# Kernel tuning notes

Measured on AMD Instinct MI355X. Metric: run time of the kernel, lower is better.

## Reference

```python
import jax, jax.numpy as jnp
import numpy as np

D_MODEL = 512
D_STATE = 128
D_CONV = 4
EXPAND = 2
HEADDIM = 64
NLAYERS = 2
D_INNER = EXPAND * D_MODEL          # 1024
NHEADS = D_INNER // HEADDIM         # 16
CONV_DIM = D_INNER + 2 * D_STATE    # 1280 (x, B, C share the depthwise conv)
D_IN_PROJ = 2 * D_INNER + 2 * D_STATE + NHEADS  # 2320 (z, xBC, dt)
VOCAB = 40
SEQ = 64
BATCH = 512
NUM_CLASSES = 2
FC_HID = 128
EPS = 1e-5


def setup_inputs() -> dict:
    key = jax.random.key(0)
    ks = jax.random.split(key, 12)
    x = jax.random.randint(ks[0], (BATCH, SEQ), 0, VOCAB)
    emb = jax.random.uniform(ks[1], (VOCAB, D_MODEL), minval=-0.1, maxval=0.1)
    emb = emb.at[0].set(0.0)  # padding_idx=0
    pos = jax.random.normal(ks[2], (1, SEQ, D_MODEL)) * 0.02
    in_proj_w = jax.random.normal(ks[3], (NLAYERS, D_IN_PROJ, D_MODEL)) * 0.02
    conv_w = jax.random.normal(ks[4], (NLAYERS, CONV_DIM, D_CONV)) * 0.1
    conv_b = jnp.zeros((NLAYERS, CONV_DIM))
    dt0 = jax.random.uniform(ks[5], (NLAYERS, NHEADS), minval=1e-3, maxval=0.1)
    dt_bias = dt0 + jnp.log(-jnp.expm1(-dt0))  # inverse softplus of dt0
    A_log = jnp.log(jax.random.uniform(ks[6], (NLAYERS, NHEADS), minval=1.0, maxval=16.0))
    D_skip = jnp.ones((NLAYERS, NHEADS))
    norm_w = jnp.ones((NLAYERS, D_INNER))
    out_proj_w = jax.random.normal(ks[7], (NLAYERS, D_MODEL, D_INNER)) * 0.02
    ln_g = jnp.ones((NLAYERS, D_MODEL))
    ln_b = jnp.zeros((NLAYERS, D_MODEL))
    fc1_w = jax.random.uniform(ks[8], (FC_HID, D_MODEL), minval=-0.1, maxval=0.1)
    fc1_b = jnp.zeros((FC_HID,))
    fc2_w = jax.random.uniform(ks[9], (NUM_CLASSES, FC_HID), minval=-0.1, maxval=0.1)
    fc2_b = jnp.zeros((NUM_CLASSES,))
    return dict(x=x, emb=emb, pos=pos, in_proj_w=in_proj_w, conv_w=conv_w,
                conv_b=conv_b, dt_bias=dt_bias, A_log=A_log, D_skip=D_skip,
                norm_w=norm_w, out_proj_w=out_proj_w, ln_g=ln_g, ln_b=ln_b,
                fc1_w=fc1_w, fc1_b=fc1_b, fc2_w=fc2_w, fc2_b=fc2_b)


def _layernorm(h, g, b):
    mu = jnp.mean(h, axis=-1, keepdims=True)
    var = jnp.mean(jnp.square(h - mu), axis=-1, keepdims=True)
    return (h - mu) * jax.lax.rsqrt(var + EPS) * g + b


def _mamba2_block(h, in_proj_w, conv_w, conv_b, dt_bias, A_log, D_skip, norm_w, out_proj_w):
    b, s, _ = h.shape
    zxbcdt = jnp.einsum('bsd,ed->bse', h, in_proj_w)  # [b,s,D_IN_PROJ]
    z = zxbcdt[..., :D_INNER]
    xBC = zxbcdt[..., D_INNER:D_INNER + CONV_DIM]
    dt_raw = zxbcdt[..., D_INNER + CONV_DIM:]          # [b,s,NHEADS]
    # causal depthwise 1D conv + silu
    xBC_t = jnp.pad(jnp.swapaxes(xBC, 1, 2), ((0, 0), (0, 0), (D_CONV - 1, 0)))
    conv = jax.lax.conv_general_dilated(xBC_t, conv_w[:, None, :], (1,), 'VALID',
                                        feature_group_count=CONV_DIM)
    xBC = jax.nn.silu(jnp.swapaxes(conv + conv_b[None, :, None], 1, 2))
    xs = xBC[..., :D_INNER].reshape(b, s, NHEADS, HEADDIM)
    Bm = xBC[..., D_INNER:D_INNER + D_STATE]           # [b,s,n] (ngroups=1)
    Cm = xBC[..., D_INNER + D_STATE:]                  # [b,s,n]
    dt = jax.nn.softplus(dt_raw + dt_bias)             # [b,s,h]
    A = -jnp.exp(A_log)                                # [h], negative
    # exact quadratic (1-semiseparable) SSD form, equal to the selective scan
    cum = jnp.cumsum(dt * A, axis=1)                   # [b,s,h]
    diff = cum[:, :, None, :] - cum[:, None, :, :]     # [b,i,j,h] <= 0 for i>=j
    causal = jnp.tril(jnp.ones((s, s), dtype=bool))
    L = jnp.exp(jnp.where(causal[None, :, :, None], diff, -jnp.inf))  # decay mask
    scores = jnp.einsum('bin,bjn->bij', Cm, Bm)
    M = scores[..., None] * L                          # [b,i,j,h]
    y = jnp.einsum('bijh,bjh,bjhp->bihp', M, dt, xs)
    y = y + D_skip[None, None, :, None] * xs
    y = y.reshape(b, s, D_INNER)
    # gated RMSNorm
    y = y * jax.nn.silu(z)
    y = y * jax.lax.rsqrt(jnp.mean(jnp.square(y), axis=-1, keepdims=True) + EPS) * norm_w
    return jnp.einsum('bsi,di->bsd', y, out_proj_w)


def reference(x, emb, pos, in_proj_w, conv_w, conv_b, dt_bias, A_log, D_skip,
              norm_w, out_proj_w, ln_g, ln_b, fc1_w, fc1_b, fc2_w, fc2_b):
    h = emb[x] + pos[:, :x.shape[1], :]  # dropout is identity in eval
    for l in range(NLAYERS):
        y = _mamba2_block(h, in_proj_w[l], conv_w[l], conv_b[l], dt_bias[l],
                          A_log[l], D_skip[l], norm_w[l], out_proj_w[l])
        h = h + _layernorm(y, ln_g[l], ln_b[l])
    pm = (jnp.sum(h, axis=-1) != 0).astype(h.dtype)[..., None]  # [b,s,1]
    pooled = jnp.sum(h * pm, axis=1) / jnp.clip(jnp.sum(pm, axis=1), 1.0, None)
    hid = jax.nn.relu(pooled @ fc1_w.T + fc1_b)
    return hid @ fc2_w.T + fc2_b
```

## Files before the change

### kernel.cpp

```cpp
#include <hip/hip_runtime.h>
#include <hip/hip_bf16.h>

#define D_MODEL   512
#define D_STATE   128
#define D_CONV    4
#define HEADDIM   64
#define NLAYERS   2
#define D_INNER   1024
#define NHEADS    16
#define CONV_DIM  1280
#define D_IN_PROJ 2320
#define NPAD      2560
#define SEQ       64
#define BATCH     512
#define NTOK      (BATCH*SEQ)
#define FC_HID    128
#define EPS       1e-5f

using bf16 = __hip_bfloat16;
typedef __bf16 bf16x8 __attribute__((ext_vector_type(8)));
typedef float  f32x4  __attribute__((ext_vector_type(4)));

__device__ __forceinline__ float b2f(bf16 v)  { return __bfloat162float(v); }
__device__ __forceinline__ bf16  f2b(float v) { return __float2bfloat16(v); }
__device__ __forceinline__ float bflo(unsigned u){ return __builtin_bit_cast(float, u << 16); }
__device__ __forceinline__ float bfhi(unsigned u){ return __builtin_bit_cast(float, u & 0xffff0000u); }

__device__ __forceinline__ void gl_lds16(const void* g, void* l) {
    __builtin_amdgcn_global_load_lds((const __attribute__((address_space(1))) void*)g,
                                     (__attribute__((address_space(3))) void*)l, 16, 0, 0);
}

__global__ __launch_bounds__(256) void k_embed(const int* __restrict__ x,
        const float* __restrict__ emb, const float* __restrict__ pos,
        float* __restrict__ h, bf16* __restrict__ hb) {
    int idx = blockIdx.x*256 + threadIdx.x;
    int d   = (idx & 127) * 4;
    int tok = idx >> 7;
    int s   = tok & (SEQ-1);
    int v   = x[tok];
    float4 e4 = *(const float4*)(emb + (size_t)v*D_MODEL + d);
    float4 p4 = *(const float4*)(pos + (size_t)s*D_MODEL + d);
    float4 r; r.x=e4.x+p4.x; r.y=e4.y+p4.y; r.z=e4.z+p4.z; r.w=e4.w+p4.w;
    *(float4*)(h + (size_t)tok*D_MODEL + d) = r;
    bf16 o[4] = { f2b(r.x), f2b(r.y), f2b(r.z), f2b(r.w) };
    *(uint2*)(hb + (size_t)tok*D_MODEL + d) = *(uint2*)&o[0];
}

__global__ __launch_bounds__(256) void k_cvtw(const float* __restrict__ src,
        bf16* __restrict__ dst, int R, int Kc, int total8) {
    int idx = blockIdx.x*256 + threadIdx.x;
    if (idx >= total8) return;
    int e0 = idx*8;
    int r = e0 / Kc, c = e0 % Kc;
    bf16 tb[8];
    if (r < R) {
        float4 f0 = *(const float4*)(src + (size_t)r*Kc + c);
        float4 f1 = *(const float4*)(src + (size_t)r*Kc + c + 4);
        tb[0]=f2b(f0.x); tb[1]=f2b(f0.y); tb[2]=f2b(f0.z); tb[3]=f2b(f0.w);
        tb[4]=f2b(f1.x); tb[5]=f2b(f1.y); tb[6]=f2b(f1.z); tb[7]=f2b(f1.w);
    } else {
        #pragma unroll
        for (int e=0;e<8;e++) tb[e] = f2b(0.f);
    }
    *(uint4*)(dst + (size_t)r*Kc + c) = *(uint4*)&tb[0];
}

__global__ __launch_bounds__(512, 1) void k_gemm256(const bf16* __restrict__ A,
        const bf16* __restrict__ B, bf16* __restrict__ zbuf,
        bf16* __restrict__ xbcc, float* __restrict__ dt, float* __restrict__ cum,
        const float* __restrict__ cw, const float* __restrict__ cb,
        const float* __restrict__ dt_bias, const float* __restrict__ A_log,
        int ctok)
{
    constexpr int KDIM = 512, NT = KDIM/64, NBX = NPAD/256;
    extern __shared__ __align__(16) char lds[];
    bf16* Cs = (bf16*)lds;

    const int nwg = gridDim.x;
    const int q = nwg >> 3, r = nwg & 7;
    const int xcd = blockIdx.x & 7, loc = blockIdx.x >> 3;
    const int wg = ((xcd < r) ? xcd*(q+1) : r*(q+1) + (xcd-r)*q) + loc;
    const int m0 = (wg / NBX) * 256;
    const int n0 = (wg % NBX) * 256;

    const int t = threadIdx.x;
    const int wid = t >> 6, lane = t & 63;
    const int lr = lane & 15, lg = lane >> 4;
    const int wm = (wid >> 2)*128, wn = (wid & 3)*64;
    const int srow = wid*32;
    const int sr   = lane >> 3;
    const int scol = ((lane & 7) ^ sr) * 8;

    const bf16* Abase = A + (size_t)(m0 + srow + sr)*KDIM + scol;
    const bf16* Bbase = B + (size_t)(n0 + srow + sr)*KDIM + scol;

    f32x4 acc[8][4] = {};
    char* bc = lds;
    char* bn = lds + 65536;

    auto STAGE = [&](char* buf, int kk) {
        #pragma unroll
        for (int c = 0; c < 4; c++) {
            gl_lds16(Abase + (size_t)(c*8)*KDIM + kk, buf + (srow + c*8)*128);
            gl_lds16(Bbase + (size_t)(c*8)*KDIM + kk, buf + 32768 + (srow + c*8)*128);
        }
    };

    STAGE(bc, 0);
    asm volatile("s_waitcnt vmcnt(0)" ::: "memory");
    __builtin_amdgcn_s_barrier();

    #pragma unroll
    for (int kt = 0; kt < NT; kt++) {
        if (kt + 1 < NT) STAGE(bn, (kt+1)*64);
        #pragma unroll
        for (int ks = 0; ks < 64; ks += 32) {
            bf16x8 a[8], b[4];
            #pragma unroll
            for (int mi=0;mi<8;mi++) {
                int ra = wm + mi*16 + lr;
                a[mi] = *(const bf16x8*)(bc + ra*128 + ((((ks>>3)+lg) ^ (ra&7))<<4));
            }
            #pragma unroll
            for (int ni=0;ni<4;ni++) {
                int rb = wn + ni*16 + lr;
                b[ni] = *(const bf16x8*)(bc + 32768 + rb*128 + ((((ks>>3)+lg) ^ (rb&7))<<4));
            }
            __builtin_amdgcn_s_setprio(1);
            #pragma unroll
            for (int mi=0;mi<8;mi++)
                #pragma unroll
                for (int ni=0;ni<4;ni++)
                    acc[mi][ni] = __builtin_amdgcn_mfma_f32_16x16x32_bf16(a[mi], b[ni], acc[mi][ni], 0,0,0);
            __builtin_amdgcn_s_setprio(0);
        }
        asm volatile("s_waitcnt vmcnt(0)" ::: "memory");
        __builtin_amdgcn_s_barrier();
        char* tb2 = bc; bc = bn; bn = tb2;
    }
    __builtin_amdgcn_sched_barrier(0);
    __syncthreads();

    #pragma unroll
    for (int mi=0;mi<8;mi++)
        #pragma unroll
        for (int ni=0;ni<4;ni++)
            #pragma unroll
            for (int rr=0;rr<4;rr++) {
                int row = wm + mi*16 + lg*4 + rr;
                int col = (wn + ni*16 + lr) ^ ((row & 7) << 3);
                Cs[row*256 + col] = f2b(acc[mi][ni][rr]);
            }
    __syncthreads();

    const int rsub = t >> 5;
    const int c8   = (t & 31) * 8;

    if (n0 < 1024) {
        #pragma unroll
        for (int it = 0; it < 16; it++) {
            int row = it*16 + rsub;
            const bf16* src = &Cs[row*256 + (c8 ^ ((row & 7) << 3))];
            *(uint4*)(zbuf + (size_t)(m0+row)*1024 + n0 + c8) = *(const uint4*)src;
        }
    } else if (n0 < 2304) {
        const int cbase = n0 - 1024 + c8;
        float4 wreg[8]; float bias[8];
        #pragma unroll
        for (int e=0;e<8;e++) wreg[e] = *(const float4*)(cw + (size_t)(cbase+e)*4);
        {
            float4 b0 = *(const float4*)(cb + cbase);
            float4 b1 = *(const float4*)(cb + cbase + 4);
            bias[0]=b0.x; bias[1]=b0.y; bias[2]=b0.z; bias[3]=b0.w;
            bias[4]=b1.x; bias[5]=b1.y; bias[6]=b1.z; bias[7]=b1.w;
        }
        #pragma unroll
        for (int it = 0; it < 16; it++) {
            int row = it*16 + rsub;
            int sl  = row & (SEQ-1);
            float m3 = (sl >= 3) ? 1.f : 0.f;
            float m2 = (sl >= 2) ? 1.f : 0.f;
            float m1 = (sl >= 1) ? 1.f : 0.f;
            const bf16* sm3 = &Cs[(row-3)*256 + (c8 ^ (((row-3) & 7) << 3))];
            const bf16* sm2 = &Cs[(row-2)*256 + (c8 ^ (((row-2) & 7) << 3))];
            const bf16* sm1 = &Cs[(row-1)*256 + (c8 ^ (((row-1) & 7) << 3))];
            const bf16* sm0 = &Cs[(row  )*256 + (c8 ^ (((row  ) & 7) << 3))];
            float a[8];
            #pragma unroll
            for (int e=0;e<8;e++) {
                a[e] = bias[e]
                     + m3 * b2f(sm3[e]) * wreg[e].x
                     + m2 * b2f(sm2[e]) * wreg[e].y
                     + m1 * b2f(sm1[e]) * wreg[e].z
                     +      b2f(sm0[e]) * wreg[e].w;
            }
            bf16 outv[8];
            #pragma unroll
            for (int e=0;e<8;e++) outv[e] = f2b(a[e] / (1.f + __expf(-a[e])));
            *(uint4*)(xbcc + (size_t)(m0+row)*CONV_DIM + cbase) = *(uint4*)&outv[0];
        }
    } else {
        for (int p = wid; p < 64; p += 8) {
            int sq = p >> 4, head = p & 15;
            int row = sq*64 + lane;
            float raw = b2f(Cs[row*256 + (head ^ ((row & 7) << 3))]) + dt_bias[head];
            float dval = (raw > 20.f) ? raw : log1pf(__expf(raw));
            float Ah = -__expf(A_log[head]);
            float cc = dval * Ah;
            #pragma unroll
            for (int o=1;o<64;o<<=1) { float v = __shfl_up(cc, o); if (lane >= o) cc += v; }
            int tok = m0 + row;
            dt [(size_t)head*ctok + tok] = dval;
            cum[(size_t)head*ctok + tok] = cc;
        }
    }
}

__global__ __launch_bounds__(256) void k_gemm128(const bf16* __restrict__ A,
        const bf16* __restrict__ B, bf16* __restrict__ C, int Nout, int nbx)
{
    constexpr int KDIM = 1024, NT = KDIM/64;
    __shared__ __align__(16) char lds[65536];
    bf16* Cs = (bf16*)lds;

    const int nwg = gridDim.x;
    const int q = nwg >> 3, r = nwg & 7;
    const int xcd = blockIdx.x & 7, loc = blockIdx.x >> 3;
    const int wg = ((xcd < r) ? xcd*(q+1) : r*(q+1) + (xcd-r)*q) + loc;
    const int m0 = (wg / nbx) * 128;
    const int n0 = (wg % nbx) * 128;

    const int t = threadIdx.x;
    const int wid = t >> 6, lane = t & 63;
    const int lr = lane & 15, lg = lane >> 4;
    const int wm = (wid >> 1)*64, wn = (wid & 1)*64;
    const int srow = wid*32;
    const int sr   = lane >> 3;
    const int scol = ((lane & 7) ^ sr) * 8;

    const bf16* Abase = A + (size_t)(m0 + srow + sr)*KDIM + scol;
    const bf16* Bbase = B + (size_t)(n0 + srow + sr)*KDIM + scol;

    f32x4 acc[4][4] = {};
    char* bc = lds;
    char* bn = lds + 32768;

    auto STAGE = [&](char* buf, int kk) {
        #pragma unroll
        for (int c = 0; c < 4; c++) {
            gl_lds16(Abase + (size_t)(c*8)*KDIM + kk, buf + (srow + c*8)*128);
            gl_lds16(Bbase + (size_t)(c*8)*KDIM + kk, buf + 16384 + (srow + c*8)*128);
        }
    };

    STAGE(bc, 0);
    asm volatile("s_waitcnt vmcnt(0)" ::: "memory");
    __builtin_amdgcn_s_barrier();

    #pragma unroll
    for (int kt = 0; kt < NT; kt++) {
        if (kt + 1 < NT) STAGE(bn, (kt+1)*64);
        #pragma unroll
        for (int ks = 0; ks < 64; ks += 32) {
            bf16x8 a[4], b[4];
            #pragma unroll
            for (int mi=0;mi<4;mi++) {
                int ra = wm + mi*16 + lr;
                a[mi] = *(const bf16x8*)(bc + ra*128 + ((((ks>>3)+lg) ^ (ra&7))<<4));
            }
            #pragma unroll
            for (int ni=0;ni<4;ni++) {
                int rb = wn + ni*16 + lr;
                b[ni] = *(const bf16x8*)(bc + 16384 + rb*128 + ((((ks>>3)+lg) ^ (rb&7))<<4));
            }
            __builtin_amdgcn_s_setprio(1);
            #pragma unroll
            for (int mi=0;mi<4;mi++)
                #pragma unroll
                for (int ni=0;ni<4;ni++)
                    acc[mi][ni] = __builtin_amdgcn_mfma_f32_16x16x32_bf16(a[mi], b[ni], acc[mi][ni], 0,0,0);
            __builtin_amdgcn_s_setprio(0);
        }
        asm volatile("s_waitcnt vmcnt(0)" ::: "memory");
        __builtin_amdgcn_s_barrier();
        char* tb2 = bc; bc = bn; bn = tb2;
    }
    __builtin_amdgcn_sched_barrier(0);

    #pragma unroll
    for (int mi=0;mi<4;mi++)
        #pragma unroll
        for (int ni=0;ni<4;ni++)
            #pragma unroll
            for (int rr=0;rr<4;rr++)
                Cs[(wm+mi*16+lg*4+rr)*136 + wn+ni*16+lr] = f2b(acc[mi][ni][rr]);
    __syncthreads();
    const int rsub = t >> 4;
    const int c8   = (t & 15) * 8;
    #pragma unroll
    for (int it = 0; it < 8; it++) {
        int row = it*16 + rsub;
        *(uint4*)(C + (size_t)(m0+row)*Nout + n0 + c8) = *(const uint4*)&Cs[row*136 + c8];
    }
}

__global__ __launch_bounds__(256) void k_ssd(const bf16* __restrict__ xbcc,
        const float* __restrict__ dt, const float* __restrict__ cum,
        const float* __restrict__ Dskip, bf16* __restrict__ y, int ctok) {
    __shared__ float scores[64][66];
    __shared__ __align__(16) bf16 Wb [64][72];
    __shared__ __align__(16) bf16 xsT[64][72];
    __shared__ __align__(16) bf16 ys [64][72];
    const int bid = blockIdx.x;
    const int b   = bid >> 1;
    const int hg  = (bid & 1) * 8;
    const int t = threadIdx.x;
    const size_t tokbase = (size_t)b*SEQ;
    const int lane = t & 63, lr = lane & 15, lg = lane >> 4;
    const int w = t >> 6;

    {
        int i0 = w*16;
        f32x4 sacc[4] = {};
        const bf16* Cbase = xbcc + tokbase*CONV_DIM + D_INNER + D_STATE;
        const bf16* Bbase = xbcc + tokbase*CONV_DIM + D_INNER;
        #pragma unroll
        for (int ks = 0; ks < D_STATE; ks += 32) {
            bf16x8 af = *(const bf16x8*)(Cbase + (size_t)(i0+lr)*CONV_DIM + ks + lg*8);
            #pragma unroll
            for (int jt = 0; jt < 4; jt++) {
                bf16x8 bfr = *(const bf16x8*)(Bbase + (size_t)(jt*16+lr)*CONV_DIM + ks + lg*8);
                sacc[jt] = __builtin_amdgcn_mfma_f32_16x16x32_bf16(af, bfr, sacc[jt], 0,0,0);
            }
        }
        #pragma unroll
        for (int jt=0;jt<4;jt++)
            #pragma unroll
            for (int rr=0;rr<4;rr++)
                scores[i0 + lg*4 + rr][jt*16 + lr] = sacc[jt][rr];
    }

    const int wi = t >> 2;
    const int wj0 = (t & 3) * 16;

    for (int hl = 0; hl < 8; hl++) {
        const int hh = hg + hl;
        const size_t cbase = (size_t)hh*ctok + tokbase;
        __syncthreads();

        #pragma unroll
        for (int cc = 0; cc < 2; cc++) {
            int ch = cc*256 + t;
            int rr = ch >> 3, c8 = (ch & 7)*8;
            uint4 v = *(const uint4*)(xbcc + (tokbase + rr)*CONV_DIM + hh*HEADDIM + c8);
            const bf16* pv = (const bf16*)&v;
            #pragma unroll
            for (int e=0;e<8;e++) xsT[c8+e][rr] = pv[e];
        }
        {
            float cum_i = cum[cbase + wi];
            float cjf[16], djf[16];
            #pragma unroll
            for (int qq=0; qq<4; qq++) {
                float4 a4 = *(const float4*)(cum + cbase + wj0 + qq*4);
                float4 d4 = *(const float4*)(dt  + cbase + wj0 + qq*4);
                cjf[qq*4+0]=a4.x; cjf[qq*4+1]=a4.y; cjf[qq*4+2]=a4.z; cjf[qq*4+3]=a4.w;
                djf[qq*4+0]=d4.x; djf[qq*4+1]=d4.y; djf[qq*4+2]=d4.z; djf[qq*4+3]=d4.w;
            }
            bf16 tb[16];
            #pragma unroll
            for (int e=0;e<16;e++) {
                int j = wj0 + e;
                float wv = (j <= wi) ? scores[wi][j] * __expf(cum_i - cjf[e]) * djf[e] : 0.f;
                tb[e] = f2b(wv);
            }
            *(uint4*)&Wb[wi][wj0]   = *(uint4*)&tb[0];
            *(uint4*)&Wb[wi][wj0+8] = *(uint4*)&tb[8];
        }
        __syncthreads();

        {
            float dsk = Dskip[hh];
            f32x4 yacc[4] = {};
            #pragma unroll
            for (int ks = 0; ks < 64; ks += 32) {
                bf16x8 a = *(const bf16x8*)&Wb[w*16 + lr][ks + lg*8];
                #pragma unroll
                for (int n=0; n<4; n++) {
                    bf16x8 bb = *(const bf16x8*)&xsT[n*16 + lr][ks + lg*8];
                    yacc[n] = __builtin_amdgcn_mfma_f32_16x16x32_bf16(a, bb, yacc[n], 0,0,0);
                }
            }
            #pragma unroll
            for (int n=0; n<4; n++)
                #pragma unroll
                for (int rr=0; rr<4; rr++) {
                    int row = w*16 + lg*4 + rr;
                    int col = n*16 + lr;
                    ys[row][col] = f2b(yacc[n][rr] + dsk * b2f(xsT[col][row]));
                }
        }
        __syncthreads();

        #pragma unroll
        for (int cc = 0; cc < 2; cc++) {
            int ch = cc*256 + t;
            int rr = ch >> 3, c8 = (ch & 7)*8;
            *(uint4*)(y + (tokbase + rr)*D_INNER + hh*HEADDIM + c8) = *(const uint4*)&ys[rr][c8];
        }
    }
}

__global__ __launch_bounds__(256) void k_gaterms(bf16* __restrict__ y,
        const bf16* __restrict__ zbuf, const float* __restrict__ nw) {
    int tok = blockIdx.x*2 + (threadIdx.x >> 7);
    int t   = threadIdx.x & 127;
    int hi  = threadIdx.x >> 7, wv = (threadIdx.x >> 6) & 1;
    __shared__ float red[2][2];
    int d = t*8;
    uint4 yv = *(const uint4*)(y    + (size_t)tok*D_INNER + d);
    uint4 zv = *(const uint4*)(zbuf + (size_t)tok*D_INNER + d);
    const unsigned* yu = (const unsigned*)&yv;
    const unsigned* zu = (const unsigned*)&zv;
    float g[8]; float ss = 0.f;
    #pragma unroll
    for (int e=0;e<4;e++) {
        float y0 = bflo(yu[e]), y1 = bfhi(yu[e]);
        float z0 = bflo(zu[e]), z1 = bfhi(zu[e]);
        float g0 = y0 * z0 / (1.f + __expf(-z0));
        float g1 = y1 * z1 / (1.f + __expf(-z1));
        g[2*e] = g0; g[2*e+1] = g1;
        ss += g0*g0 + g1*g1;
    }
    for (int o=32;o>0;o>>=1) ss += __shfl_down(ss, o);
    if ((threadIdx.x & 63) == 0) red[hi][wv] = ss;
    __syncthreads();
    float scale = rsqrtf((red[hi][0]+red[hi][1])/(float)D_INNER + EPS);
    bf16 outv[8];
    #pragma unroll
    for (int e=0;e<8;e++) outv[e] = f2b(g[e] * scale * nw[d+e]);
    *(uint4*)(y + (size_t)tok*D_INNER + d) = *(uint4*)&outv[0];
}

__global__ __launch_bounds__(256) void k_resln(float* __restrict__ h,
        bf16* __restrict__ hb, const bf16* __restrict__ tmp,
        const float* __restrict__ g, const float* __restrict__ bb) {
    int tok = blockIdx.x*2 + (threadIdx.x >> 7);
    int t   = threadIdx.x & 127;
    int hi  = threadIdx.x >> 7, wv = (threadIdx.x >> 6) & 1;
    __shared__ float redS[2][2], redQ[2][2];
    int d = t*4;
    uint2 u2 = *(const uint2*)(tmp + (size_t)tok*D_MODEL + d);
    const unsigned* uu = (const unsigned*)&u2;
    float v0 = bflo(uu[0]), v1 = bfhi(uu[0]), v2 = bflo(uu[1]), v3 = bfhi(uu[1]);
    float s = v0+v1+v2+v3;
    float qq = v0*v0+v1*v1+v2*v2+v3*v3;
    for (int o=32;o>0;o>>=1){ s += __shfl_down(s,o); qq += __shfl_down(qq,o); }
    if ((threadIdx.x & 63) == 0){ redS[hi][wv]=s; redQ[hi][wv]=qq; }
    __syncthreads();
    float S = redS[hi][0]+redS[hi][1];
    float Q = redQ[hi][0]+redQ[hi][1];
    float mu  = S/(float)D_MODEL;
    float var = Q/(float)D_MODEL - mu*mu;
    float inv = rsqrtf(var + EPS);
    size_t base = (size_t)tok*D_MODEL + d;
    float4 h4 = *(const float4*)(h + base);
    float4 g4 = *(const float4*)(g + d);
    float4 b4 = *(const float4*)(bb + d);
    h4.x += (v0-mu)*inv*g4.x + b4.x;
    h4.y += (v1-mu)*inv*g4.y + b4.y;
    h4.z += (v2-mu)*inv*g4.z + b4.z;
    h4.w += (v3-mu)*inv*g4.w + b4.w;
    *(float4*)(h + base) = h4;
    bf16 o4[4] = { f2b(h4.x), f2b(h4.y), f2b(h4.z), f2b(h4.w) };
    *(uint2*)(hb + base) = *(uint2*)&o4[0];
}

__global__ __launch_bounds__(256) void k_pool(const float* __restrict__ h,
        float* __restrict__ pooled) {
    int b = blockIdx.x, t = threadIdx.x;
    __shared__ float ps[64][4];
    __shared__ float pm[64];
    __shared__ float cntS;
    {
        int s = t >> 2, qq = t & 3;
        const float4* row = (const float4*)(h + ((size_t)b*SEQ + s)*D_MODEL + qq*128);
        float acc = 0;
        #pragma unroll 8
        for (int e=0;e<32;e++) { float4 f = row[e]; acc += f.x+f.y+f.z+f.w; }
        ps[s][qq] = acc;
    }
    __syncthreads();
    if (t < 64) pm[t] = (ps[t][0]+ps[t][1]+ps[t][2]+ps[t][3]) != 0.f ? 1.f : 0.f;
    __syncthreads();
    if (t == 0) { float c=0; for (int s2=0;s2<64;s2++) c+=pm[s2]; cntS = fmaxf(c,1.f); }
    __syncthreads();
    float cnt = cntS;
    #pragma unroll
    for (int rep=0;rep<2;rep++) {
        int d = t + rep*256;
        float acc = 0;
        for (int s2=0;s2<64;s2++) acc += h[((size_t)b*SEQ+s2)*D_MODEL + d] * pm[s2];
        pooled[(size_t)b*D_MODEL + d] = acc / cnt;
    }
}

__global__ __launch_bounds__(128) void k_fc(const float* __restrict__ pooled,
        const float* __restrict__ w1, const float* __restrict__ b1,
        const float* __restrict__ w2, const float* __restrict__ b2,
        float* __restrict__ out) {
    int b = blockIdx.x, j = threadIdx.x;
    __shared__ float hid[FC_HID];
    const float* p  = pooled + (size_t)b*D_MODEL;
    const float* wr = w1 + (size_t)j*D_MODEL;
    float acc = b1[j];
    for (int d=0; d<D_MODEL; d+=4)
        acc += p[d]*wr[d] + p[d+1]*wr[d+1] + p[d+2]*wr[d+2] + p[d+3]*wr[d+3];
    hid[j] = fmaxf(acc, 0.f);
    __syncthreads();
    if (j < 2) {
        float o = b2[j];
        for (int k=0;k<FC_HID;k++) o += hid[k]*w2[j*FC_HID+k];
        out[b*2 + j] = o;
    }
}

extern "C" void kernel_launch(void* const* d_in, const int* in_sizes, int n_in,
                              void* d_out, int out_size, void* d_ws, size_t ws_size,
                              hipStream_t stream) {
    (void)in_sizes; (void)n_in; (void)out_size;
    const int*   x        = (const int*)  d_in[0];
    const float* emb      = (const float*)d_in[1];
    const float* pos      = (const float*)d_in[2];
    const float* in_proj  = (const float*)d_in[3];
    const float* conv_w   = (const float*)d_in[4];
    const float* conv_b   = (const float*)d_in[5];
    const float* dt_bias  = (const float*)d_in[6];
    const float* A_log    = (const float*)d_in[7];
    const float* D_skip   = (const float*)d_in[8];
    const float* norm_w   = (const float*)d_in[9];
    const float* out_proj = (const float*)d_in[10];
    const float* ln_g     = (const float*)d_in[11];
    const float* ln_b     = (const float*)d_in[12];
    const float* fc1_w    = (const float*)d_in[13];
    const float* fc1_b    = (const float*)d_in[14];
    const float* fc2_w    = (const float*)d_in[15];
    const float* fc2_b    = (const float*)d_in[16];
    float* out = (float*)d_out;

    (void)hipFuncSetAttribute((const void*)k_gemm256,
            hipFuncAttributeMaxDynamicSharedMemorySize, 131072);

    const size_t H_B   = (size_t)NTOK * D_MODEL * 4;
    const size_t HB_B  = (size_t)NTOK * D_MODEL * 2;
    const size_t WPI_B = (size_t)NPAD * D_MODEL * 2;
    const size_t WPO_B = (size_t)D_MODEL * D_INNER * 2;
    const size_t PBASE = H_B + HB_B + NLAYERS*(WPI_B + WPO_B);

    const size_t PER_TOK = 2048 + 2560 + 2048 + 128;
    int CB = BATCH;
    while (CB > 8 && PBASE + (size_t)CB*SEQ*PER_TOK > ws_size) CB >>= 1;
    const int CT = CB * SEQ;
    const int NC = BATCH / CB;

    char* ws = (char*)d_ws;
    float* h    = (float*)(ws);
    bf16*  hb   = (bf16*) (ws + H_B);
    bf16*  wpi  = (bf16*) (ws + H_B + HB_B);
    bf16*  wpo  = (bf16*) (ws + H_B + HB_B + NLAYERS*WPI_B);
    char*  tr   = ws + PBASE;
    bf16*  zbuf = (bf16*) (tr);
    bf16*  xbcc = (bf16*) (tr + (size_t)CT*2048);
    bf16*  ybuf = (bf16*) (tr + (size_t)CT*(2048+2560));
    float* dt   = (float*)(tr + (size_t)CT*(2048+2560+2048));
    float* cum  = dt + (size_t)CT*NHEADS;
    bf16*  tmp  = xbcc;
    float* pooled = (float*)tr;

    for (int l = 0; l < NLAYERS; l++) {
        int t8i = NPAD*D_MODEL/8;
        k_cvtw<<<(t8i+255)/256, 256, 0, stream>>>(in_proj + (size_t)l*D_IN_PROJ*D_MODEL,
                wpi + (size_t)l*NPAD*D_MODEL, D_IN_PROJ, D_MODEL, t8i);
        int t8o = D_MODEL*D_INNER/8;
        k_cvtw<<<(t8o+255)/256, 256, 0, stream>>>(out_proj + (size_t)l*D_MODEL*D_INNER,
                wpo + (size_t)l*D_MODEL*D_INNER, D_MODEL, D_INNER, t8o);
    }

    k_embed<<<(NTOK*128)/256, 256, 0, stream>>>(x, emb, pos, h, hb);

    const int NBX_O = D_MODEL/128;

    for (int l = 0; l < NLAYERS; l++) {
        const bf16* wi = wpi + (size_t)l*NPAD*D_MODEL;
        const bf16* wo = wpo + (size_t)l*D_MODEL*D_INNER;
        for (int c = 0; c < NC; c++) {
            const int tok0 = c * CT;
            float* hc  = h  + (size_t)tok0 * D_MODEL;
            bf16*  hbc = hb + (size_t)tok0 * D_MODEL;
            k_gemm256<<<(CT/256)*(NPAD/256), 512, 131072, stream>>>(hbc, wi, zbuf,
                    xbcc, dt, cum,
                    conv_w + (size_t)l*CONV_DIM*D_CONV, conv_b + (size_t)l*CONV_DIM,
                    dt_bias + l*NHEADS, A_log + l*NHEADS, CT);
            k_ssd<<<CB*2, 256, 0, stream>>>(xbcc, dt, cum, D_skip + l*NHEADS, ybuf, CT);
            k_gaterms<<<CT/2, 256, 0, stream>>>(ybuf, zbuf, norm_w + (size_t)l*D_INNER);
            k_gemm128<<<(CT/128)*NBX_O, 256, 0, stream>>>(ybuf, wo, tmp, D_MODEL, NBX_O);
            k_resln<<<CT/2, 256, 0, stream>>>(hc, hbc, tmp, ln_g + l*D_MODEL, ln_b + l*D_MODEL);
        }
    }

    k_pool<<<BATCH, 256, 0, stream>>>(h, pooled);
    k_fc<<<BATCH, FC_HID, 0, stream>>>(pooled, fc1_w, fc1_b, fc2_w, fc2_b, out);
}
```

Before: 670.5 us.

## Use 4-stage LDS ring with 32-wide K tiles in both GEMMs

Both GEMM kernels drop the double-buffered 64-wide K tiles with a full vmcnt(0) drain each iteration. They now use a four-buffer ring of 32-wide K tiles, keeping three tiles in flight and waiting only on the oldest with partial vmcnt counts. The aim is to hide global-to-LDS latency better and avoid stalling on every load. In exchange there are twice as many barriers per K, a new 4-way XOR swizzle on 64-byte rows, and an added syncthreads before the epilogue that reuses LDS.

```diff
diff --git a/kernel.cpp b/kernel.cpp
--- a/kernel.cpp
+++ b/kernel.cpp
@@ -31,6 +31,12 @@
                                      (__attribute__((address_space(3))) void*)l, 16, 0, 0);
 }
 
+__device__ __forceinline__ void wait_tiles(int rem) {
+    if (rem >= 2)      asm volatile("s_waitcnt vmcnt(8)" ::: "memory");
+    else if (rem == 1) asm volatile("s_waitcnt vmcnt(4)" ::: "memory");
+    else               asm volatile("s_waitcnt vmcnt(0)" ::: "memory");
+}
+
 __global__ __launch_bounds__(256) void k_embed(const int* __restrict__ x,
         const float* __restrict__ emb, const float* __restrict__ pos,
         float* __restrict__ h, bf16* __restrict__ hb) {
@@ -73,7 +79,7 @@
         const float* __restrict__ dt_bias, const float* __restrict__ A_log,
         int ctok)
 {
-    constexpr int KDIM = 512, NT = KDIM/64, NBX = NPAD/256;
+    constexpr int KDIM = 512, NT = KDIM/32, NBX = NPAD/256;
     extern __shared__ __align__(16) char lds[];
     bf16* Cs = (bf16*)lds;
 
@@ -88,56 +94,49 @@
     const int wid = t >> 6, lane = t & 63;
     const int lr = lane & 15, lg = lane >> 4;
     const int wm = (wid >> 2)*128, wn = (wid & 3)*64;
-    const int srow = wid*32;
-    const int sr   = lane >> 3;
-    const int scol = ((lane & 7) ^ sr) * 8;
-
-    const bf16* Abase = A + (size_t)(m0 + srow + sr)*KDIM + scol;
-    const bf16* Bbase = B + (size_t)(n0 + srow + sr)*KDIM + scol;
+    const int sr4 = lane >> 2;
+    const int sc4 = ((lane & 3) ^ (sr4 & 3)) * 8;
+
+    const bf16* Abase = A + (size_t)(m0 + wid*32 + sr4)*KDIM + sc4;
+    const bf16* Bbase = B + (size_t)(n0 + wid*32 + sr4)*KDIM + sc4;
 
     f32x4 acc[8][4] = {};
-    char* bc = lds;
-    char* bn = lds + 65536;
-
-    auto STAGE = [&](char* buf, int kk) {
-        #pragma unroll
-        for (int c = 0; c < 4; c++) {
-            gl_lds16(Abase + (size_t)(c*8)*KDIM + kk, buf + (srow + c*8)*128);
-            gl_lds16(Bbase + (size_t)(c*8)*KDIM + kk, buf + 32768 + (srow + c*8)*128);
+
+    auto STAGE = [&](int bi, int kk) {
+        char* buf = lds + bi*32768;
+        #pragma unroll
+        for (int c = 0; c < 2; c++) {
+            gl_lds16(Abase + (size_t)(c*16)*KDIM + kk, buf + (wid*32 + c*16)*64);
+            gl_lds16(Bbase + (size_t)(c*16)*KDIM + kk, buf + 16384 + (wid*32 + c*16)*64);
         }
     };
 
-    STAGE(bc, 0);
-    asm volatile("s_waitcnt vmcnt(0)" ::: "memory");
-    __builtin_amdgcn_s_barrier();
+    STAGE(0, 0); STAGE(1, 32); STAGE(2, 64);
 
     #pragma unroll
     for (int kt = 0; kt < NT; kt++) {
-        if (kt + 1 < NT) STAGE(bn, (kt+1)*64);
-        #pragma unroll
-        for (int ks = 0; ks < 64; ks += 32) {
-            bf16x8 a[8], b[4];
-            #pragma unroll
-            for (int mi=0;mi<8;mi++) {
-                int ra = wm + mi*16 + lr;
-                a[mi] = *(const bf16x8*)(bc + ra*128 + ((((ks>>3)+lg) ^ (ra&7))<<4));
-            }
-            #pragma unroll
-            for (int ni=0;ni<4;ni++) {
-                int rb = wn + ni*16 + lr;
-                b[ni] = *(const bf16x8*)(bc + 32768 + rb*128 + ((((ks>>3)+lg) ^ (rb&7))<<4));
-            }
-            __builtin_amdgcn_s_setprio(1);
-            #pragma unroll
-            for (int mi=0;mi<8;mi++)
-                #pragma unroll
-                for (int ni=0;ni<4;ni++)
-                    acc[mi][ni] = __builtin_amdgcn_mfma_f32_16x16x32_bf16(a[mi], b[ni], acc[mi][ni], 0,0,0);
-            __builtin_amdgcn_s_setprio(0);
-        }
-        asm volatile("s_waitcnt vmcnt(0)" ::: "memory");
+        wait_tiles(NT - 1 - kt);
         __builtin_amdgcn_s_barrier();
-        char* tb2 = bc; bc = bn; bn = tb2;
+        if (kt + 3 < NT) STAGE((kt+3) & 3, (kt+3)*32);
+        char* bc = lds + (kt & 3)*32768;
+        bf16x8 a[8], b[4];
+        #pragma unroll
+        for (int mi=0;mi<8;mi++) {
+            int ra = wm + mi*16 + lr;
+            a[mi] = *(const bf16x8*)(bc + ra*64 + ((lg ^ (ra&3))<<4));
+        }
+        #pragma unroll
+        for (int ni=0;ni<4;ni++) {
+            int rb = wn + ni*16 + lr;
+            b[ni] = *(const bf16x8*)(bc + 16384 + rb*64 + ((lg ^ (rb&3))<<4));
+        }
+        __builtin_amdgcn_s_setprio(1);
+        #pragma unroll
+        for (int mi=0;mi<8;mi++)
+            #pragma unroll
+            for (int ni=0;ni<4;ni++)
+                acc[mi][ni] = __builtin_amdgcn_mfma_f32_16x16x32_bf16(a[mi], b[ni], acc[mi][ni], 0,0,0);
+        __builtin_amdgcn_s_setprio(0);
     }
     __builtin_amdgcn_sched_barrier(0);
     __syncthreads();
@@ -220,7 +219,7 @@
 __global__ __launch_bounds__(256) void k_gemm128(const bf16* __restrict__ A,
         const bf16* __restrict__ B, bf16* __restrict__ C, int Nout, int nbx)
 {
-    constexpr int KDIM = 1024, NT = KDIM/64;
+    constexpr int KDIM = 1024, NT = KDIM/32;
     __shared__ __align__(16) char lds[65536];
     bf16* Cs = (bf16*)lds;
 
@@ -235,58 +234,52 @@
     const int wid = t >> 6, lane = t & 63;
     const int lr = lane & 15, lg = lane >> 4;
     const int wm = (wid >> 1)*64, wn = (wid & 1)*64;
-    const int srow = wid*32;
-    const int sr   = lane >> 3;
-    const int scol = ((lane & 7) ^ sr) * 8;
-
-    const bf16* Abase = A + (size_t)(m0 + srow + sr)*KDIM + scol;
-    const bf16* Bbase = B + (size_t)(n0 + srow + sr)*KDIM + scol;
+    const int sr4 = lane >> 2;
+    const int sc4 = ((lane & 3) ^ (sr4 & 3)) * 8;
+
+    const bf16* Abase = A + (size_t)(m0 + wid*32 + sr4)*KDIM + sc4;
+    const bf16* Bbase = B + (size_t)(n0 + wid*32 + sr4)*KDIM + sc4;
 
     f32x4 acc[4][4] = {};
-    char* bc = lds;
-    char* bn = lds + 32768;
-
-    auto STAGE = [&](char* buf, int kk) {
-        #pragma unroll
-        for (int c = 0; c < 4; c++) {
-            gl_lds16(Abase + (size_t)(c*8)*KDIM + kk, buf + (srow + c*8)*128);
-            gl_lds16(Bbase + (size_t)(c*8)*KDIM + kk, buf + 16384 + (srow + c*8)*128);
+
+    auto STAGE = [&](int bi, int kk) {
+        char* buf = lds + bi*16384;
+        #pragma unroll
+        for (int c = 0; c < 2; c++) {
+            gl_lds16(Abase + (size_t)(c*16)*KDIM + kk, buf + (wid*32 + c*16)*64);
+            gl_lds16(Bbase + (size_t)(c*16)*KDIM + kk, buf + 8192 + (wid*32 + c*16)*64);
         }
     };
 
-    STAGE(bc, 0);
-    asm volatile("s_waitcnt vmcnt(0)" ::: "memory");
-    __builtin_amdgcn_s_barrier();
+    STAGE(0, 0); STAGE(1, 32); STAGE(2, 64);
 
     #pragma unroll
     for (int kt = 0; kt < NT; kt++) {
-        if (kt + 1 < NT) STAGE(bn, (kt+1)*64);
-        #pragma unroll
-        for (int ks = 0; ks < 64; ks += 32) {
-            bf16x8 a[4], b[4];
-            #pragma unroll
-            for (int mi=0;mi<4;mi++) {
-                int ra = wm + mi*16 + lr;
-                a[mi] = *(const bf16x8*)(bc + ra*128 + ((((ks>>3)+lg) ^ (ra&7))<<4));
-            }
-            #pragma unroll
-            for (int ni=0;ni<4;ni++) {
-                int rb = wn + ni*16 + lr;
-                b[ni] = *(const bf16x8*)(bc + 16384 + rb*128 + ((((ks>>3)+lg) ^ (rb&7))<<4));
-            }
-            __builtin_amdgcn_s_setprio(1);
-            #pragma unroll
-            for (int mi=0;mi<4;mi++)
-                #pragma unroll
-                for (int ni=0;ni<4;ni++)
-                    acc[mi][ni] = __builtin_amdgcn_mfma_f32_16x16x32_bf16(a[mi], b[ni], acc[mi][ni], 0,0,0);
-            __builtin_amdgcn_s_setprio(0);
-        }
-        asm volatile("s_waitcnt vmcnt(0)" ::: "memory");
+        wait_tiles(NT - 1 - kt);
         __builtin_amdgcn_s_barrier();
-        char* tb2 = bc; bc = bn; bn = tb2;
+        if (kt + 3 < NT) STAGE((kt+3) & 3, (kt+3)*32);
+        char* bc = lds + (kt & 3)*16384;
+        bf16x8 a[4], b[4];
+        #pragma unroll
+        for (int mi=0;mi<4;mi++) {
+            int ra = wm + mi*16 + lr;
+            a[mi] = *(const bf16x8*)(bc + ra*64 + ((lg ^ (ra&3))<<4));
+        }
+        #pragma unroll
+        for (int ni=0;ni<4;ni++) {
+            int rb = wn + ni*16 + lr;
+            b[ni] = *(const bf16x8*)(bc + 8192 + rb*64 + ((lg ^ (rb&3))<<4));
+        }
+        __builtin_amdgcn_s_setprio(1);
+        #pragma unroll
+        for (int mi=0;mi<4;mi++)
+            #pragma unroll
+            for (int ni=0;ni<4;ni++)
+                acc[mi][ni] = __builtin_amdgcn_mfma_f32_16x16x32_bf16(a[mi], b[ni], acc[mi][ni], 0,0,0);
+        __builtin_amdgcn_s_setprio(0);
     }
     __builtin_amdgcn_sched_barrier(0);
+    __syncthreads();
 
     #pragma unroll
     for (int mi=0;mi<4;mi++)
```

New measurement: 708.0 us. +5.6%, slower.
